# Optimization experiments

Hardware: AMD Instinct MI355X
Metric: run time of the kernel (lower is better)

Reference implementation:

```python
import jax, jax.numpy as jnp
import numpy as np

N_VERTICES = 50000
N_FEATURES = 128
N_EDGES = 640000


def setup_inputs() -> dict:
    key = jax.random.key(0)
    k1, k2, k3, k4 = jax.random.split(key, 4)
    inp = jax.random.normal(k1, (N_VERTICES, N_FEATURES), dtype=jnp.float32)
    eidx = jax.random.randint(k2, (2, N_EDGES), 0, N_VERTICES, dtype=jnp.int64)
    enorm = jax.random.uniform(k3, (N_EDGES,), dtype=jnp.float32)
    esgn = jnp.sign(jax.random.normal(k4, (N_EDGES,), dtype=jnp.float32))
    return {"input": inp, "eidx": eidx, "enorm": enorm, "esgn": esgn}


def reference(input, eidx, enorm, esgn):
    sidx, tidx = eidx[0], eidx[1]
    # gather source node features, scale by signed normalized edge weight
    message = input[sidx] * (esgn * enorm)[:, None]  # [n_edges, d]
    # scatter-add messages onto target nodes
    res = jax.ops.segment_sum(message, tidx, num_segments=input.shape[0])
    return res
```

## Files before the change

### kernel.cpp

```cpp
#include <hip/hip_runtime.h>
#include <hip/hip_fp16.h>


#define N_V 50000
#define N_F 128
#define N_E 640000
#define CAP 64

#define SCAT_CHUNKS (N_E / 256)
#define SCAT_BLKS   (SCAT_CHUNKS * 8)
#define CVT_BLKS    (N_V * N_F / 8 / 256)
#define CNT_STRIDE  6272

typedef float f32x4 __attribute__((ext_vector_type(4)));

__global__ void __launch_bounds__(256) gc_prep(
    const int* __restrict__ sidx, const int* __restrict__ tidx,
    const float* __restrict__ enorm, const float* __restrict__ esgn,
    const float* __restrict__ input,
    int* __restrict__ cnt2, unsigned int* __restrict__ bucket,
    __half* __restrict__ tab)
{
    if (blockIdx.x < SCAT_BLKS) {
        const int chunk = blockIdx.x >> 3;
        const int myres = blockIdx.x & 7;
        const int e = chunk * 256 + threadIdx.x;
        const int t = tidx[e];
        if ((t & 7) == myres) {
            const int s = sidx[e];
            const float w = esgn[e] * enorm[e];
            const int pos = atomicAdd(&cnt2[myres * CNT_STRIDE + (t >> 3)], 1);
            if (pos < CAP) {
                const unsigned rec =
                    ((unsigned)__half_as_ushort(__float2half_rn(w)) << 16)
                    | (unsigned)s;
                bucket[(size_t)t * CAP + pos] = rec;
            }
        }
    } else {
        const size_t i = (size_t)(blockIdx.x - SCAT_BLKS) * 256 + threadIdx.x;
        const size_t base = i * 8;
        const f32x4 a = *reinterpret_cast<const f32x4*>(input + base);
        const f32x4 b = *reinterpret_cast<const f32x4*>(input + base + 4);
        uint4 pk;
        pk.x = (unsigned)__half_as_ushort(__float2half_rn(a.x))
             | ((unsigned)__half_as_ushort(__float2half_rn(a.y)) << 16);
        pk.y = (unsigned)__half_as_ushort(__float2half_rn(a.z))
             | ((unsigned)__half_as_ushort(__float2half_rn(a.w)) << 16);
        pk.z = (unsigned)__half_as_ushort(__float2half_rn(b.x))
             | ((unsigned)__half_as_ushort(__float2half_rn(b.y)) << 16);
        pk.w = (unsigned)__half_as_ushort(__float2half_rn(b.z))
             | ((unsigned)__half_as_ushort(__float2half_rn(b.w)) << 16);
        *reinterpret_cast<uint4*>(tab + base) = pk;
    }
}

__global__ void __launch_bounds__(256) gc_gather_h(
    const __half* __restrict__ tab, const int* __restrict__ cnt2,
    const unsigned int* __restrict__ bucket, float* __restrict__ out)
{
    const int v = blockIdx.x * 4 + (threadIdx.x >> 6);
    if (v >= N_V) return;
    const int lane  = threadIdx.x & 63;
    const int half_ = lane >> 5;
    const int q     = (lane & 31) * 4;

    const int n = min(cnt2[(v & 7) * CNT_STRIDE + (v >> 3)], CAP);
    unsigned rec = 0;
    if (lane < n)
        rec = __builtin_nontemporal_load(bucket + (size_t)v * CAP + lane);
    const int   rs = (int)(rec & 0xffffu);
    const float rw = __half2float(__ushort_as_half((unsigned short)(rec >> 16)));

    f32x4 acc = (f32x4)0.f;
    const int nIter = (n + 1) >> 1;
    int k = 0;
    for (; k + 2 <= nIter; k += 2) {
        const int i0 = 2 * k + half_;
        const int i1 = 2 * k + 2 + half_;
        const int   s0 = __shfl(rs, i0);
        const float w0 = __shfl(rw, i0);
        const int   s1 = __shfl(rs, i1);
        const float w1 = __shfl(rw, i1);
        const uint2 u0 = *reinterpret_cast<const uint2*>(tab + (size_t)s0 * N_F + q);
        const uint2 u1 = *reinterpret_cast<const uint2*>(tab + (size_t)s1 * N_F + q);
        const float2 a0 = __half22float2(*reinterpret_cast<const __half2*>(&u0.x));
        const float2 b0 = __half22float2(*reinterpret_cast<const __half2*>(&u0.y));
        const float2 a1 = __half22float2(*reinterpret_cast<const __half2*>(&u1.x));
        const float2 b1 = __half22float2(*reinterpret_cast<const __half2*>(&u1.y));
        acc.x += a0.x * w0; acc.y += a0.y * w0; acc.z += b0.x * w0; acc.w += b0.y * w0;
        acc.x += a1.x * w1; acc.y += a1.y * w1; acc.z += b1.x * w1; acc.w += b1.y * w1;
    }
    if (k < nIter) {
        const int i0 = 2 * k + half_;
        const int   s0 = __shfl(rs, i0);
        const float w0 = __shfl(rw, i0);
        const uint2 u0 = *reinterpret_cast<const uint2*>(tab + (size_t)s0 * N_F + q);
        const float2 a0 = __half22float2(*reinterpret_cast<const __half2*>(&u0.x));
        const float2 b0 = __half22float2(*reinterpret_cast<const __half2*>(&u0.y));
        acc.x += a0.x * w0; acc.y += a0.y * w0; acc.z += b0.x * w0; acc.w += b0.y * w0;
    }

    acc.x += __shfl(acc.x, lane + 32);
    acc.y += __shfl(acc.y, lane + 32);
    acc.z += __shfl(acc.z, lane + 32);
    acc.w += __shfl(acc.w, lane + 32);

    if (half_ == 0) {
        __builtin_nontemporal_store(acc,
            reinterpret_cast<f32x4*>(out + (size_t)v * N_F + q));
    }
}

__global__ void __launch_bounds__(256) gc_atomic_fallback(
    const float* __restrict__ input, const int* __restrict__ sidx,
    const int* __restrict__ tidx, const float* __restrict__ enorm,
    const float* __restrict__ esgn, float* __restrict__ out)
{
    const int e = blockIdx.x * 8 + (threadIdx.x >> 5);
    if (e >= N_E) return;
    const int lane = threadIdx.x & 31;
    const int s = sidx[e], t = tidx[e];
    const float w = esgn[e] * enorm[e];
    float4 v = reinterpret_cast<const float4*>(input + (size_t)s * N_F)[lane];
    float* orow = out + (size_t)t * N_F + lane * 4;
    atomicAdd(orow + 0, v.x * w);
    atomicAdd(orow + 1, v.y * w);
    atomicAdd(orow + 2, v.z * w);
    atomicAdd(orow + 3, v.w * w);
}

extern "C" void kernel_launch(void* const* d_in, const int* in_sizes, int n_in,
                              void* d_out, int out_size, void* d_ws, size_t ws_size,
                              hipStream_t stream) {
    const float* input = (const float*)d_in[0];
    const int*   eidx  = (const int*)d_in[1];
    const float* enorm = (const float*)d_in[2];
    const float* esgn  = (const float*)d_in[3];
    float* out = (float*)d_out;

    const int* sidx = eidx;
    const int* tidx = eidx + N_E;

    const size_t need = (size_t)8 * CNT_STRIDE * sizeof(int)
                      + (size_t)N_V * CAP * sizeof(unsigned int)
                      + (size_t)N_V * N_F * sizeof(__half);

    if (ws_size >= need) {
        int*          cnt2   = (int*)d_ws;
        unsigned int* bucket = (unsigned int*)(cnt2 + 8 * CNT_STRIDE);
        __half*       tab    = (__half*)(bucket + (size_t)N_V * CAP);
        hipMemsetAsync(cnt2, 0, (size_t)8 * CNT_STRIDE * sizeof(int), stream);
        hipLaunchKernelGGL(gc_prep, dim3(SCAT_BLKS + CVT_BLKS), dim3(256),
                           0, stream, sidx, tidx, enorm, esgn, input,
                           cnt2, bucket, tab);
        hipLaunchKernelGGL(gc_gather_h, dim3((N_V + 3) / 4), dim3(256),
                           0, stream, tab, cnt2, bucket, out);
    } else {
        hipMemsetAsync(d_out, 0, (size_t)out_size * sizeof(float), stream);
        hipLaunchKernelGGL(gc_atomic_fallback, dim3(N_E / 8), dim3(256), 0,
                           stream, input, sidx, tidx, enorm, esgn, out);
    }
}
```

Baseline: 142.2 us.

## Fuse fp16 conversion into scatter blocks and widen gather loads to 16 bytes

The prep kernel no longer launches separate conversion blocks. Every scatter block also converts 320 floats of the input table to fp16, with the load issued before the atomic bucketing and the store after it so the two overlap. The gather kernel now splits each wavefront into four groups of 16 lanes, each lane reading 8 halves (16 bytes) per edge and handling 8 edges per iteration, then reduces across the groups with xor shuffles. This cuts the launched block count and the number of load instructions, at the cost of more registers and wasted edge slots when a vertex has few neighbours.

Result: faster. 135.9 us (-4.5%).

```diff
diff --git a/kernel.cpp b/kernel.cpp
--- a/kernel.cpp
+++ b/kernel.cpp
@@ -9,7 +9,7 @@
 
 #define SCAT_CHUNKS (N_E / 256)
 #define SCAT_BLKS   (SCAT_CHUNKS * 8)
-#define CVT_BLKS    (N_V * N_F / 8 / 256)
+#define CVT_PER_BLK 320
 #define CNT_STRIDE  6272
 
 typedef float f32x4 __attribute__((ext_vector_type(4)));
@@ -21,28 +21,18 @@
     int* __restrict__ cnt2, unsigned int* __restrict__ bucket,
     __half* __restrict__ tab)
 {
-    if (blockIdx.x < SCAT_BLKS) {
-        const int chunk = blockIdx.x >> 3;
-        const int myres = blockIdx.x & 7;
-        const int e = chunk * 256 + threadIdx.x;
-        const int t = tidx[e];
-        if ((t & 7) == myres) {
-            const int s = sidx[e];
-            const float w = esgn[e] * enorm[e];
-            const int pos = atomicAdd(&cnt2[myres * CNT_STRIDE + (t >> 3)], 1);
-            if (pos < CAP) {
-                const unsigned rec =
-                    ((unsigned)__half_as_ushort(__float2half_rn(w)) << 16)
-                    | (unsigned)s;
-                bucket[(size_t)t * CAP + pos] = rec;
-            }
-        }
-    } else {
-        const size_t i = (size_t)(blockIdx.x - SCAT_BLKS) * 256 + threadIdx.x;
-        const size_t base = i * 8;
-        const f32x4 a = *reinterpret_cast<const f32x4*>(input + base);
-        const f32x4 b = *reinterpret_cast<const f32x4*>(input + base + 4);
-        uint4 pk;
+    const int chunk = blockIdx.x >> 3;
+    const int myres = blockIdx.x & 7;
+    const int e = chunk * 256 + threadIdx.x;
+    const int t = tidx[e];
+
+    uint4 pk;
+    size_t cbase = 0;
+    const bool do_cvt = (threadIdx.x < (CVT_PER_BLK / 8));
+    if (do_cvt) {
+        cbase = (size_t)blockIdx.x * CVT_PER_BLK + (size_t)threadIdx.x * 8;
+        const f32x4 a = *reinterpret_cast<const f32x4*>(input + cbase);
+        const f32x4 b = *reinterpret_cast<const f32x4*>(input + cbase + 4);
         pk.x = (unsigned)__half_as_ushort(__float2half_rn(a.x))
              | ((unsigned)__half_as_ushort(__float2half_rn(a.y)) << 16);
         pk.y = (unsigned)__half_as_ushort(__float2half_rn(a.z))
@@ -51,7 +41,22 @@
              | ((unsigned)__half_as_ushort(__float2half_rn(b.y)) << 16);
         pk.w = (unsigned)__half_as_ushort(__float2half_rn(b.z))
              | ((unsigned)__half_as_ushort(__float2half_rn(b.w)) << 16);
-        *reinterpret_cast<uint4*>(tab + base) = pk;
+    }
+
+    if ((t & 7) == myres) {
+        const int s = sidx[e];
+        const float w = esgn[e] * enorm[e];
+        const int pos = atomicAdd(&cnt2[myres * CNT_STRIDE + (t >> 3)], 1);
+        if (pos < CAP) {
+            const unsigned rec =
+                ((unsigned)__half_as_ushort(__float2half_rn(w)) << 16)
+                | (unsigned)s;
+            bucket[(size_t)t * CAP + pos] = rec;
+        }
+    }
+
+    if (do_cvt) {
+        *reinterpret_cast<uint4*>(tab + cbase) = pk;
     }
 }
 
@@ -62,8 +67,9 @@
     const int v = blockIdx.x * 4 + (threadIdx.x >> 6);
     if (v >= N_V) return;
     const int lane  = threadIdx.x & 63;
-    const int half_ = lane >> 5;
-    const int q     = (lane & 31) * 4;
+    const int quart = lane >> 4;
+    const int l16   = lane & 15;
+    const int q     = l16 * 8;
 
     const int n = min(cnt2[(v & 7) * CNT_STRIDE + (v >> 3)], CAP);
     unsigned rec = 0;
@@ -72,43 +78,48 @@
     const int   rs = (int)(rec & 0xffffu);
     const float rw = __half2float(__ushort_as_half((unsigned short)(rec >> 16)));
 
-    f32x4 acc = (f32x4)0.f;
-    const int nIter = (n + 1) >> 1;
-    int k = 0;
-    for (; k + 2 <= nIter; k += 2) {
-        const int i0 = 2 * k + half_;
-        const int i1 = 2 * k + 2 + half_;
+    f32x4 accA = (f32x4)0.f;
+    f32x4 accB = (f32x4)0.f;
+    const int nIter = (n + 7) >> 3;
+    for (int it = 0; it < nIter; ++it) {
+        const int i0 = it * 8 + quart;
+        const int i1 = i0 + 4;
         const int   s0 = __shfl(rs, i0);
         const float w0 = __shfl(rw, i0);
         const int   s1 = __shfl(rs, i1);
         const float w1 = __shfl(rw, i1);
-        const uint2 u0 = *reinterpret_cast<const uint2*>(tab + (size_t)s0 * N_F + q);
-        const uint2 u1 = *reinterpret_cast<const uint2*>(tab + (size_t)s1 * N_F + q);
+        const uint4 u0 = *reinterpret_cast<const uint4*>(tab + (size_t)s0 * N_F + q);
+        const uint4 u1 = *reinterpret_cast<const uint4*>(tab + (size_t)s1 * N_F + q);
         const float2 a0 = __half22float2(*reinterpret_cast<const __half2*>(&u0.x));
-        const float2 b0 = __half22float2(*reinterpret_cast<const __half2*>(&u0.y));
-        const float2 a1 = __half22float2(*reinterpret_cast<const __half2*>(&u1.x));
+        const float2 a1 = __half22float2(*reinterpret_cast<const __half2*>(&u0.y));
+        const float2 a2 = __half22float2(*reinterpret_cast<const __half2*>(&u0.z));
+        const float2 a3 = __half22float2(*reinterpret_cast<const __half2*>(&u0.w));
+        accA.x += a0.x * w0; accA.y += a0.y * w0; accA.z += a1.x * w0; accA.w += a1.y * w0;
+        accB.x += a2.x * w0; accB.y += a2.y * w0; accB.z += a3.x * w0; accB.w += a3.y * w0;
+        const float2 b0 = __half22float2(*reinterpret_cast<const __half2*>(&u1.x));
         const float2 b1 = __half22float2(*reinterpret_cast<const __half2*>(&u1.y));
-        acc.x += a0.x * w0; acc.y += a0.y * w0; acc.z += b0.x * w0; acc.w += b0.y * w0;
-        acc.x += a1.x * w1; acc.y += a1.y * w1; acc.z += b1.x * w1; acc.w += b1.y * w1;
-    }
-    if (k < nIter) {
-        const int i0 = 2 * k + half_;
-        const int   s0 = __shfl(rs, i0);
-        const float w0 = __shfl(rw, i0);
-        const uint2 u0 = *reinterpret_cast<const uint2*>(tab + (size_t)s0 * N_F + q);
-        const float2 a0 = __half22float2(*reinterpret_cast<const __half2*>(&u0.x));
-        const float2 b0 = __half22float2(*reinterpret_cast<const __half2*>(&u0.y));
-        acc.x += a0.x * w0; acc.y += a0.y * w0; acc.z += b0.x * w0; acc.w += b0.y * w0;
+        const float2 b2 = __half22float2(*reinterpret_cast<const __half2*>(&u1.z));
+        const float2 b3 = __half22float2(*reinterpret_cast<const __half2*>(&u1.w));
+        accA.x += b0.x * w1; accA.y += b0.y * w1; accA.z += b1.x * w1; accA.w += b1.y * w1;
+        accB.x += b2.x * w1; accB.y += b2.y * w1; accB.z += b3.x * w1; accB.w += b3.y * w1;
     }
 
-    acc.x += __shfl(acc.x, lane + 32);
-    acc.y += __shfl(acc.y, lane + 32);
-    acc.z += __shfl(acc.z, lane + 32);
-    acc.w += __shfl(acc.w, lane + 32);
+    #pragma unroll
+    for (int off = 16; off <= 32; off <<= 1) {
+        accA.x += __shfl_xor(accA.x, off);
+        accA.y += __shfl_xor(accA.y, off);
+        accA.z += __shfl_xor(accA.z, off);
+        accA.w += __shfl_xor(accA.w, off);
+        accB.x += __shfl_xor(accB.x, off);
+        accB.y += __shfl_xor(accB.y, off);
+        accB.z += __shfl_xor(accB.z, off);
+        accB.w += __shfl_xor(accB.w, off);
+    }
 
-    if (half_ == 0) {
-        __builtin_nontemporal_store(acc,
-            reinterpret_cast<f32x4*>(out + (size_t)v * N_F + q));
+    if (quart == 0) {
+        float* orow = out + (size_t)v * N_F + q;
+        __builtin_nontemporal_store(accA, reinterpret_cast<f32x4*>(orow));
+        __builtin_nontemporal_store(accB, reinterpret_cast<f32x4*>(orow + 4));
     }
 }
 
@@ -151,7 +162,7 @@
         unsigned int* bucket = (unsigned int*)(cnt2 + 8 * CNT_STRIDE);
         __half*       tab    = (__half*)(bucket + (size_t)N_V * CAP);
         hipMemsetAsync(cnt2, 0, (size_t)8 * CNT_STRIDE * sizeof(int), stream);
-        hipLaunchKernelGGL(gc_prep, dim3(SCAT_BLKS + CVT_BLKS), dim3(256),
+        hipLaunchKernelGGL(gc_prep, dim3(SCAT_BLKS), dim3(256),
                            0, stream, sidx, tidx, enorm, esgn, input,
                            cnt2, bucket, tab);
         hipLaunchKernelGGL(gc_gather_h, dim3((N_V + 3) / 4), dim3(256),
```
